# Optimization experiments

Hardware: AMD Instinct MI355X
Metric: run time of the kernel (lower is better)

## Reference

```python
import jax, jax.numpy as jnp
import numpy as np

N = 50000   # nodes
E = 800000  # edges (avg degree 16)
D = 64      # in_feat
OUT = 64    # out_feat


def _layernorm(x, gamma, beta, eps=1e-5):
    m = jnp.mean(x, axis=-1, keepdims=True)
    v = jnp.mean((x - m) ** 2, axis=-1, keepdims=True)  # biased var, as torch LayerNorm
    return (x - m) * jax.lax.rsqrt(v + eps) * gamma + beta


def setup_inputs() -> dict:
    key = jax.random.key(0)
    ks = jax.random.split(key, 6)
    s1 = 1.0 / np.sqrt(D)
    s2 = 1.0 / np.sqrt(2 * D)
    return {
        "x": jax.random.normal(ks[0], (N, D), dtype=jnp.float32),
        "edge_index": jax.random.randint(ks[1], (2, E), 0, N, dtype=jnp.int64),
        "W1a": jax.random.normal(ks[2], (D, D), dtype=jnp.float32) * s1,
        "W1b": jax.random.normal(ks[3], (D, D), dtype=jnp.float32) * s1,
        "gamma1": jnp.ones((D,), jnp.float32),
        "beta1": jnp.zeros((D,), jnp.float32),
        "w": jnp.ones((D,), jnp.float32),
        "gamma2": jnp.ones((D,), jnp.float32),
        "beta2": jnp.zeros((D,), jnp.float32),
        "W2a": jax.random.normal(ks[4], (D, 2 * D), dtype=jnp.float32) * s2,
        "W2b": jax.random.normal(ks[5], (OUT, D), dtype=jnp.float32) * s1,
    }


def reference(x, edge_index, W1a, W1b, gamma1, beta1, w, gamma2, beta2, W2a, W2b):
    row, col = edge_index[0], edge_index[1]
    n = x.shape[0]
    # gather -> MLP1 (two bias-free linears with ReLU)
    msg = x[row]                                        # [E, D]
    msg = jax.nn.relu(msg @ W1a.T) @ W1b.T              # [E, D]
    # scatter_mean over destination nodes
    s = jax.ops.segment_sum(msg, col, num_segments=n)   # [N, D]
    cnt = jax.ops.segment_sum(jnp.ones((col.shape[0],), x.dtype), col, num_segments=n)
    agg = s / jnp.maximum(cnt, 1.0)[:, None]
    agg = _layernorm(agg, gamma1, beta1)
    # repulsion + residual + LayerNorm
    fx = _layernorm(x + (x - agg) * w, gamma2, beta2)
    # concat -> MLP2
    h = jnp.concatenate([fx, agg], axis=1)              # [N, 2D]
    return jax.nn.relu(h @ W2a.T) @ W2b.T               # [N, OUT]
```

## Files before the change

kernel.cpp:

```cpp
#include <hip/hip_runtime.h>
#include <hip/hip_bf16.h>

#define NN 50000
#define NE 800000
#define CAP 48
#define BINS 3125
#define HROW 3126
#define P1B 391
#define CHUNK 2048
#define MLPB 768
#define SUPT 782
#define HIDX(b) ((b) + ((b) >> 4))

typedef short v8s __attribute__((ext_vector_type(8)));
typedef float v4f __attribute__((ext_vector_type(4)));
#define MFMA16(a, b, c) __builtin_amdgcn_mfma_f32_16x16x32_bf16(a, b, c, 0, 0, 0)

__device__ __forceinline__ float bfu2f(unsigned short u) {
    union { unsigned int i; float f; } v; v.i = ((unsigned int)u) << 16; return v.f;
}
__device__ __forceinline__ unsigned short f2bf_rne(float f) {
    union { float f; unsigned int i; } v; v.f = f;
    unsigned int x = v.i;
    unsigned int r = x + 0x7fffu + ((x >> 16) & 1u);
    return (unsigned short)(r >> 16);
}
__device__ __forceinline__ v8s fragf32(const float* p) {
    float4 u = ((const float4*)p)[0];
    float4 v = ((const float4*)p)[1];
    v8s r;
    r[0] = (short)f2bf_rne(u.x); r[1] = (short)f2bf_rne(u.y);
    r[2] = (short)f2bf_rne(u.z); r[3] = (short)f2bf_rne(u.w);
    r[4] = (short)f2bf_rne(v.x); r[5] = (short)f2bf_rne(v.y);
    r[6] = (short)f2bf_rne(v.z); r[7] = (short)f2bf_rne(v.w);
    return r;
}
__device__ __forceinline__ v8s fragbf(const unsigned short* p) {
    union { uint4 u; v8s s; } t; t.u = *((const uint4*)p); return t.s;
}
__device__ __forceinline__ v4f vzero() { v4f z; z[0]=0.f; z[1]=0.f; z[2]=0.f; z[3]=0.f; return z; }

__global__ __launch_bounds__(256) void p1fat_k(const int* __restrict__ ei,
                                               const float* __restrict__ x,
                                               const float* __restrict__ W1a,
                                               const float* __restrict__ W1b,
                                               unsigned int* __restrict__ chunkbuf,
                                               unsigned short* __restrict__ histT,
                                               unsigned short* __restrict__ y) {
    __shared__ __align__(16) unsigned int smem[8448];
    int t = threadIdx.x;
    if (blockIdx.x < P1B) {
        unsigned int*   hcnt  = smem;
        unsigned short* sst16 = (unsigned short*)(smem + 4352);
        unsigned int*   data  = smem + 4352 + 2048;
        unsigned int*   scan  = data;
        int pc = blockIdx.x;
        int e0 = pc * CHUNK;
        int e1 = e0 + CHUNK; if (e1 > NE) e1 = NE;
        int ne = e1 - e0;
        bool i64 = ((ei[1] | ei[3] | ei[5] | ei[7]) == 0);
        for (int i = t; i < 4352; i += 256) hcnt[i] = 0;
        __syncthreads();
        unsigned int packed[8];
#pragma unroll
        for (int i = 0; i < 8; ++i) {
            int e = e0 + t + 256 * i;
            unsigned int pk = 0xFFFFFFFFu;
            if (e < e1) {
                int col = i64 ? ei[2 * (NE + e)] : ei[NE + e];
                int row = i64 ? ei[2 * e]        : ei[e];
                pk = ((unsigned int)col << 16) | (unsigned int)row;
                atomicAdd(&hcnt[HIDX(col >> 4)], 1u);
            }
            packed[i] = pk;
        }
        __syncthreads();
        unsigned int vv[16], tsum = 0;
#pragma unroll
        for (int k = 0; k < 16; ++k) { vv[k] = hcnt[HIDX(16 * t + k)]; tsum += vv[k]; }
        scan[t] = tsum;
        __syncthreads();
        for (int off = 1; off < 256; off <<= 1) {
            unsigned int a = (t >= off) ? scan[t - off] : 0;
            __syncthreads();
            scan[t] += a;
            __syncthreads();
        }
        {
            unsigned int run = scan[t] - tsum;
#pragma unroll
            for (int k = 0; k < 16; ++k) {
                int bb = 16 * t + k;
                hcnt[HIDX(bb)] = run;
                sst16[bb] = (unsigned short)run;
                run += vv[k];
            }
        }
        __syncthreads();
#pragma unroll
        for (int i = 0; i < 8; ++i) {
            unsigned int pk = packed[i];
            if (pk != 0xFFFFFFFFu) {
                unsigned int pos = atomicAdd(&hcnt[HIDX(pk >> 20)], 1u);
                data[pos] = pk;
            }
        }
        __syncthreads();
        unsigned int* cb = chunkbuf + (size_t)pc * CHUNK;
        for (int i = t; i < ne; i += 256) cb[i] = data[i];
        unsigned short* hrow = histT + (size_t)pc * HROW;
        for (int i = t; i < BINS; i += 256) hrow[i] = sst16[i];
        if (t == 0) hrow[BINS] = (unsigned short)ne;
        return;
    }
    unsigned short* wa  = (unsigned short*)smem;
    unsigned short* wb  = wa + 64 * 72;
    unsigned short* h1s = wb + 64 * 72;
    for (int i = t; i < 64 * 64; i += 256) {
        int r = i >> 6, c = i & 63;
        wa[r * 72 + c] = f2bf_rne(W1a[i]);
        wb[r * 72 + c] = f2bf_rne(W1b[i]);
    }
    __syncthreads();
    int w = t >> 6, l = t & 63;
    int lm = l & 15, lq = l >> 4;
    for (int st = blockIdx.x - P1B; st < SUPT; st += MLPB) {
        int nb = st * 64;
        int arow = nb + w * 16 + lm;
        int arc = arow < NN ? arow : NN - 1;
        const float* xr = x + (size_t)arc * 64;
        v8s a0 = fragf32(xr + lq * 8);
        v8s a1 = fragf32(xr + 32 + lq * 8);
        v4f acc[4];
#pragma unroll
        for (int jt = 0; jt < 4; ++jt) acc[jt] = vzero();
#pragma unroll
        for (int jt = 0; jt < 4; ++jt) {
            const unsigned short* wr = &wa[(jt * 16 + lm) * 72];
            acc[jt] = MFMA16(a0, fragbf(wr + lq * 8), acc[jt]);
            acc[jt] = MFMA16(a1, fragbf(wr + 32 + lq * 8), acc[jt]);
        }
#pragma unroll
        for (int jt = 0; jt < 4; ++jt)
#pragma unroll
            for (int r = 0; r < 4; ++r)
                h1s[(w * 16 + lq * 4 + r) * 72 + jt * 16 + lm] = f2bf_rne(fmaxf(acc[jt][r], 0.0f));
        __syncthreads();
        v8s c0 = fragbf(&h1s[(w * 16 + lm) * 72 + lq * 8]);
        v8s c1 = fragbf(&h1s[(w * 16 + lm) * 72 + 32 + lq * 8]);
        v4f acc2[4];
#pragma unroll
        for (int jt = 0; jt < 4; ++jt) acc2[jt] = vzero();
#pragma unroll
        for (int jt = 0; jt < 4; ++jt) {
            const unsigned short* wr = &wb[(jt * 16 + lm) * 72];
            acc2[jt] = MFMA16(c0, fragbf(wr + lq * 8), acc2[jt]);
            acc2[jt] = MFMA16(c1, fragbf(wr + 32 + lq * 8), acc2[jt]);
        }
#pragma unroll
        for (int jt = 0; jt < 4; ++jt)
#pragma unroll
            for (int r = 0; r < 4; ++r) {
                int n = nb + w * 16 + lq * 4 + r;
                if (n < NN) y[(size_t)n * 64 + jt * 16 + lm] = f2bf_rne(acc2[jt][r]);
            }
        __syncthreads();
    }
}

__device__ __forceinline__ float wsum64(float v) {
#pragma unroll
    for (int o = 32; o > 0; o >>= 1) v += __shfl_xor(v, o, 64);
    return v;
}
__device__ __forceinline__ void ln_store(float s0, float s1, int tdeg, int n, int p, int j, int f0,
                                         const float* __restrict__ x,
                                         const float* __restrict__ g1, const float* __restrict__ b1,
                                         const float* __restrict__ wrep,
                                         const float* __restrict__ g2, const float* __restrict__ b2,
                                         unsigned short* hrow) {
    float inv = 1.0f / (float)(tdeg > 1 ? tdeg : 1);
    float a0 = s0 * inv, a1 = s1 * inv;
    float m = wsum64(a0 + a1) * (1.0f / 128.0f);
    float d0 = a0 - m, d1 = a1 - m;
    float var = wsum64(d0 * d0 + d1 * d1) * (1.0f / 128.0f);
    float r = rsqrtf(var + 1e-5f);
    float2 g1v = *(const float2*)(g1 + f0);
    float2 b1v = *(const float2*)(b1 + f0);
    a0 = d0 * r * g1v.x + b1v.x;
    a1 = d1 * r * g1v.y + b1v.y;
    float2 xv = *(const float2*)(x + (size_t)n * 64 + f0);
    float2 wv = *(const float2*)(wrep + f0);
    float t0 = xv.x + (xv.x - a0) * wv.x;
    float t1 = xv.y + (xv.y - a1) * wv.y;
    float m2 = wsum64(t0 + t1) * (1.0f / 128.0f);
    float e0 = t0 - m2, e1 = t1 - m2;
    float var2 = wsum64(e0 * e0 + e1 * e1) * (1.0f / 128.0f);
    float r2 = rsqrtf(var2 + 1e-5f);
    float2 g2v = *(const float2*)(g2 + f0);
    float2 b2v = *(const float2*)(b2 + f0);
    float fx0 = e0 * r2 * g2v.x + b2v.x;
    float fx1 = e1 * r2 * g2v.y + b2v.y;
    unsigned* hw = (unsigned*)hrow;
    if (p == 0) hw[j]      = (unsigned)f2bf_rne(fx0) | ((unsigned)f2bf_rne(fx1) << 16);
    else        hw[32 + j] = (unsigned)f2bf_rne(a0)  | ((unsigned)f2bf_rne(a1)  << 16);
}

__global__ __launch_bounds__(256) void p2gm_k(const unsigned int* __restrict__ chunkbuf,
                                              const unsigned short* __restrict__ histT,
                                              const unsigned short* __restrict__ y,
                                              const float* __restrict__ x,
                                              const float* __restrict__ g1, const float* __restrict__ b1,
                                              const float* __restrict__ wrep,
                                              const float* __restrict__ g2, const float* __restrict__ b2,
                                              const float* __restrict__ W2a,
                                              const float* __restrict__ W2b,
                                              float* __restrict__ out) {
    __shared__ __align__(16) unsigned int k2s[9368];
    unsigned short* wa2 = (unsigned short*)k2s;
    unsigned short* wb2 = wa2 + 64 * 136;
    unsigned short* t2s = wb2 + 64 * 72;
    unsigned short* hs  = t2s + 16 * 72;
    unsigned short* dl  = hs + 16 * 136;
    unsigned int*   cl     = k2s + 8704;
    unsigned int*   scan   = cl + 16;
    unsigned short* sstart = (unsigned short*)(scan + 256);
    unsigned short* sbase  = sstart + 392;
    int t = threadIdx.x;
    int b = blockIdx.x;
    int n0g = b * 16;
    for (int i = t; i < 64 * 128; i += 256) {
        int r = i >> 7, c = i & 127;
        wa2[r * 136 + c] = f2bf_rne(W2a[i]);
    }
    for (int i = t; i < 64 * 64; i += 256) {
        int r = i >> 6, c = i & 63;
        wb2[r * 72 + c] = f2bf_rne(W2b[i]);
    }
    if (t < 16) cl[t] = 0;
    for (int i = t; i < 16 * CAP / 2; i += 256) ((unsigned int*)dl)[i] = 0;
    unsigned l0 = 0, l1 = 0;
    int s0 = 2 * t, s1 = 2 * t + 1;
    if (s0 < P1B) {
        unsigned st = histT[(size_t)s0 * HROW + b], en = histT[(size_t)s0 * HROW + b + 1];
        l0 = en - st; sstart[s0] = (unsigned short)st;
    }
    if (s1 < P1B) {
        unsigned st = histT[(size_t)s1 * HROW + b], en = histT[(size_t)s1 * HROW + b + 1];
        l1 = en - st; sstart[s1] = (unsigned short)st;
    }
    unsigned psum = l0 + l1;
    scan[t] = psum;
    __syncthreads();
    for (int off = 1; off < 256; off <<= 1) {
        unsigned a = (t >= off) ? scan[t - off] : 0;
        __syncthreads();
        scan[t] += a;
        __syncthreads();
    }
    {
        unsigned excl = scan[t] - psum;
        if (s0 < P1B) sbase[s0] = (unsigned short)excl;
        if (s1 < P1B) sbase[s1] = (unsigned short)(excl + l0);
    }
    __syncthreads();
    int tot = (int)scan[255];
    for (int k = t; k < tot; k += 256) {
        int lo = 0, hi = P1B - 1;
#pragma unroll
        for (int it = 0; it < 9; ++it) {
            int mid = (lo + hi + 1) >> 1;
            if ((int)sbase[mid] <= k) lo = mid; else hi = mid - 1;
        }
        int idx = (int)sstart[lo] + (k - (int)sbase[lo]);
        unsigned d = chunkbuf[(size_t)lo * CHUNK + idx];
        int c = (int)(d >> 16) - n0g;
        unsigned slot = atomicAdd(&cl[c], 1u);
        if (slot < CAP) dl[c * CAP + slot] = (unsigned short)(d & 0xffffu);
    }
    __syncthreads();
    int w = t >> 6, l = t & 63;
    int p = l >> 5, j = l & 31, f0 = 2 * j;
#pragma unroll
    for (int q = 0; q < 2; ++q) {
        int nl0 = q * 8 + w * 2, nl1 = nl0 + 1;
        int dA = (int)cl[nl0], dB = (int)cl[nl1];
        int eA = dA < CAP ? dA : CAP;
        int eB = dB < CAP ? dB : CAP;
        float sA0 = 0.f, sA1 = 0.f, sB0 = 0.f, sB1 = 0.f;
#pragma unroll
        for (int c6 = 0; c6 < 6; ++c6) {
            bool cA = c6 * 8 < eA, cB = c6 * 8 < eB;
            if (cA | cB) {
#pragma unroll
                for (int i = 0; i < 4; ++i) {
                    int e = c6 * 8 + 2 * i + p;
                    int idA = (int)dl[nl0 * CAP + e];
                    int idB = (int)dl[nl1 * CAP + e];
                    unsigned uA = *(const unsigned*)(y + (size_t)idA * 64 + f0);
                    unsigned uB = *(const unsigned*)(y + (size_t)idB * 64 + f0);
                    bool okA = cA && e < eA, okB = cB && e < eB;
                    sA0 += okA ? bfu2f((unsigned short)(uA & 0xffffu)) : 0.0f;
                    sA1 += okA ? bfu2f((unsigned short)(uA >> 16)) : 0.0f;
                    sB0 += okB ? bfu2f((unsigned short)(uB & 0xffffu)) : 0.0f;
                    sB1 += okB ? bfu2f((unsigned short)(uB >> 16)) : 0.0f;
                }
            }
        }
        sA0 += __shfl_xor(sA0, 32, 64);
        sA1 += __shfl_xor(sA1, 32, 64);
        sB0 += __shfl_xor(sB0, 32, 64);
        sB1 += __shfl_xor(sB1, 32, 64);
        ln_store(sA0, sA1, dA, n0g + nl0, p, j, f0, x, g1, b1, wrep, g2, b2, hs + nl0 * 136);
        ln_store(sB0, sB1, dB, n0g + nl1, p, j, f0, x, g1, b1, wrep, g2, b2, hs + nl1 * 136);
    }
    __syncthreads();
    int lm = l & 15, lq = l >> 4;
    const unsigned short* fr = hs + lm * 136;
    v8s a0 = fragbf(fr + lq * 8);
    v8s a1 = fragbf(fr + 32 + lq * 8);
    v8s a2 = fragbf(fr + 64 + lq * 8);
    v8s a3 = fragbf(fr + 96 + lq * 8);
    v4f acc = vzero();
    {
        const unsigned short* wr = &wa2[(w * 16 + lm) * 136];
        acc = MFMA16(a0, fragbf(wr + lq * 8), acc);
        acc = MFMA16(a1, fragbf(wr + 32 + lq * 8), acc);
        acc = MFMA16(a2, fragbf(wr + 64 + lq * 8), acc);
        acc = MFMA16(a3, fragbf(wr + 96 + lq * 8), acc);
    }
#pragma unroll
    for (int r = 0; r < 4; ++r)
        t2s[(lq * 4 + r) * 72 + w * 16 + lm] = f2bf_rne(fmaxf(acc[r], 0.0f));
    __syncthreads();
    v8s c0f = fragbf(&t2s[lm * 72 + lq * 8]);
    v8s c1f = fragbf(&t2s[lm * 72 + 32 + lq * 8]);
    v4f acc2 = vzero();
    {
        const unsigned short* wr = &wb2[(w * 16 + lm) * 72];
        acc2 = MFMA16(c0f, fragbf(wr + lq * 8), acc2);
        acc2 = MFMA16(c1f, fragbf(wr + 32 + lq * 8), acc2);
    }
#pragma unroll
    for (int r = 0; r < 4; ++r)
        out[(size_t)(n0g + lq * 4 + r) * 64 + w * 16 + lm] = acc2[r];
}

extern "C" void kernel_launch(void* const* d_in, const int* in_sizes, int n_in,
                              void* d_out, int out_size, void* d_ws, size_t ws_size,
                              hipStream_t stream) {
    const float* x   = (const float*)d_in[0];
    const int*   ei  = (const int*)d_in[1];
    const float* W1a = (const float*)d_in[2];
    const float* W1b = (const float*)d_in[3];
    const float* g1  = (const float*)d_in[4];
    const float* b1  = (const float*)d_in[5];
    const float* w   = (const float*)d_in[6];
    const float* g2  = (const float*)d_in[7];
    const float* b2  = (const float*)d_in[8];
    const float* W2a = (const float*)d_in[9];
    const float* W2b = (const float*)d_in[10];

    char* ws = (char*)d_ws;
    unsigned short* y        = (unsigned short*)(ws + 0);
    unsigned int*   chunkbuf = (unsigned int*)(ws + 6400000);
    unsigned short* histT    = (unsigned short*)(ws + 9603072);

    p1fat_k<<<P1B + MLPB, 256, 0, stream>>>(ei, x, W1a, W1b, chunkbuf, histT, y);
    p2gm_k<<<BINS, 256, 0, stream>>>(chunkbuf, histT, y, x, g1, b1, w, g2, b2,
                                     W2a, W2b, (float*)d_out);
    (void)in_sizes; (void)n_in; (void)out_size; (void)ws_size;
}
```

Before: 152.5 us.

## Split gather+LayerNorm from MLP2 into a separate persistent MFMA kernel

The fused gather/LayerNorm/MLP2 kernel is split in two. The first kernel writes the bf16 concatenated features h, laid out as [N,128], into the output buffer. A second persistent kernel with 768 blocks loads and converts the W2a/W2b weights once per block, then runs both MLP2 matmuls over 64-row tiles, writing fp32 results in place over h. This removes the per-block weight conversion across 3125 blocks and the large LDS footprint from the gather kernel, which should raise its occupancy. The cost is an extra launch and a round trip of h through global memory, and the in-place aliasing relies on each tile reading its own rows before any write.

```diff
diff --git a/kernel.cpp b/kernel.cpp
--- a/kernel.cpp
+++ b/kernel.cpp
@@ -178,7 +178,7 @@
                                          const float* __restrict__ g1, const float* __restrict__ b1,
                                          const float* __restrict__ wrep,
                                          const float* __restrict__ g2, const float* __restrict__ b2,
-                                         unsigned short* hrow) {
+                                         unsigned short* __restrict__ h) {
     float inv = 1.0f / (float)(tdeg > 1 ? tdeg : 1);
     float a0 = s0 * inv, a1 = s1 * inv;
     float m = wsum64(a0 + a1) * (1.0f / 128.0f);
@@ -201,44 +201,30 @@
     float2 b2v = *(const float2*)(b2 + f0);
     float fx0 = e0 * r2 * g2v.x + b2v.x;
     float fx1 = e1 * r2 * g2v.y + b2v.y;
-    unsigned* hw = (unsigned*)hrow;
+    unsigned* hw = (unsigned*)(h + (size_t)n * 128);
     if (p == 0) hw[j]      = (unsigned)f2bf_rne(fx0) | ((unsigned)f2bf_rne(fx1) << 16);
     else        hw[32 + j] = (unsigned)f2bf_rne(a0)  | ((unsigned)f2bf_rne(a1)  << 16);
 }
 
-__global__ __launch_bounds__(256) void p2gm_k(const unsigned int* __restrict__ chunkbuf,
+__global__ __launch_bounds__(256) void p2gl_k(const unsigned int* __restrict__ chunkbuf,
                                               const unsigned short* __restrict__ histT,
                                               const unsigned short* __restrict__ y,
                                               const float* __restrict__ x,
                                               const float* __restrict__ g1, const float* __restrict__ b1,
                                               const float* __restrict__ wrep,
                                               const float* __restrict__ g2, const float* __restrict__ b2,
-                                              const float* __restrict__ W2a,
-                                              const float* __restrict__ W2b,
-                                              float* __restrict__ out) {
-    __shared__ __align__(16) unsigned int k2s[9368];
-    unsigned short* wa2 = (unsigned short*)k2s;
-    unsigned short* wb2 = wa2 + 64 * 136;
-    unsigned short* t2s = wb2 + 64 * 72;
-    unsigned short* hs  = t2s + 16 * 72;
-    unsigned short* dl  = hs + 16 * 136;
-    unsigned int*   cl     = k2s + 8704;
-    unsigned int*   scan   = cl + 16;
-    unsigned short* sstart = (unsigned short*)(scan + 256);
+                                              unsigned short* __restrict__ h) {
+    __shared__ __align__(16) unsigned int s[1048];
+    unsigned short* dl     = (unsigned short*)s;
+    unsigned int*   cl     = s + 384;
+    unsigned int*   scan   = s + 400;
+    unsigned short* sstart = (unsigned short*)(s + 656);
     unsigned short* sbase  = sstart + 392;
     int t = threadIdx.x;
     int b = blockIdx.x;
     int n0g = b * 16;
-    for (int i = t; i < 64 * 128; i += 256) {
-        int r = i >> 7, c = i & 127;
-        wa2[r * 136 + c] = f2bf_rne(W2a[i]);
-    }
-    for (int i = t; i < 64 * 64; i += 256) {
-        int r = i >> 6, c = i & 63;
-        wb2[r * 72 + c] = f2bf_rne(W2b[i]);
-    }
     if (t < 16) cl[t] = 0;
-    for (int i = t; i < 16 * CAP / 2; i += 256) ((unsigned int*)dl)[i] = 0;
+    for (int i = t; i < 384; i += 256) s[i] = 0;
     unsigned l0 = 0, l1 = 0;
     int s0 = 2 * t, s1 = 2 * t + 1;
     if (s0 < P1B) {
@@ -311,39 +297,77 @@
         sA1 += __shfl_xor(sA1, 32, 64);
         sB0 += __shfl_xor(sB0, 32, 64);
         sB1 += __shfl_xor(sB1, 32, 64);
-        ln_store(sA0, sA1, dA, n0g + nl0, p, j, f0, x, g1, b1, wrep, g2, b2, hs + nl0 * 136);
-        ln_store(sB0, sB1, dB, n0g + nl1, p, j, f0, x, g1, b1, wrep, g2, b2, hs + nl1 * 136);
-    }
-    __syncthreads();
+        ln_store(sA0, sA1, dA, n0g + nl0, p, j, f0, x, g1, b1, wrep, g2, b2, h);
+        ln_store(sB0, sB1, dB, n0g + nl1, p, j, f0, x, g1, b1, wrep, g2, b2, h);
+    }
+}
+
+__global__ __launch_bounds__(256) void mlp2_k(const unsigned short* hin,
+                                              const float* __restrict__ W2a,
+                                              const float* __restrict__ W2b,
+                                              float* out) {
+    __shared__ unsigned short sm2[64 * 136 + 64 * 72 + 64 * 72];
+    unsigned short* wa2 = sm2;
+    unsigned short* wb2 = wa2 + 64 * 136;
+    unsigned short* t2s = wb2 + 64 * 72;
+    int t = threadIdx.x;
+    for (int i = t; i < 64 * 128; i += 256) {
+        int r = i >> 7, c = i & 127;
+        wa2[r * 136 + c] = f2bf_rne(W2a[i]);
+    }
+    for (int i = t; i < 64 * 64; i += 256) {
+        int r = i >> 6, c = i & 63;
+        wb2[r * 72 + c] = f2bf_rne(W2b[i]);
+    }
+    __syncthreads();
+    int w = t >> 6, l = t & 63;
     int lm = l & 15, lq = l >> 4;
-    const unsigned short* fr = hs + lm * 136;
-    v8s a0 = fragbf(fr + lq * 8);
-    v8s a1 = fragbf(fr + 32 + lq * 8);
-    v8s a2 = fragbf(fr + 64 + lq * 8);
-    v8s a3 = fragbf(fr + 96 + lq * 8);
-    v4f acc = vzero();
-    {
-        const unsigned short* wr = &wa2[(w * 16 + lm) * 136];
-        acc = MFMA16(a0, fragbf(wr + lq * 8), acc);
-        acc = MFMA16(a1, fragbf(wr + 32 + lq * 8), acc);
-        acc = MFMA16(a2, fragbf(wr + 64 + lq * 8), acc);
-        acc = MFMA16(a3, fragbf(wr + 96 + lq * 8), acc);
-    }
-#pragma unroll
-    for (int r = 0; r < 4; ++r)
-        t2s[(lq * 4 + r) * 72 + w * 16 + lm] = f2bf_rne(fmaxf(acc[r], 0.0f));
-    __syncthreads();
-    v8s c0f = fragbf(&t2s[lm * 72 + lq * 8]);
-    v8s c1f = fragbf(&t2s[lm * 72 + 32 + lq * 8]);
-    v4f acc2 = vzero();
-    {
-        const unsigned short* wr = &wb2[(w * 16 + lm) * 72];
-        acc2 = MFMA16(c0f, fragbf(wr + lq * 8), acc2);
-        acc2 = MFMA16(c1f, fragbf(wr + 32 + lq * 8), acc2);
-    }
-#pragma unroll
-    for (int r = 0; r < 4; ++r)
-        out[(size_t)(n0g + lq * 4 + r) * 64 + w * 16 + lm] = acc2[r];
+    for (int st = blockIdx.x; st < SUPT; st += MLPB) {
+        int nb = st * 64;
+        int arow = nb + w * 16 + lm;
+        int arc = arow < NN ? arow : NN - 1;
+        const unsigned short* fr = hin + (size_t)arc * 128;
+        v8s a0 = fragbf(fr + lq * 8);
+        v8s a1 = fragbf(fr + 32 + lq * 8);
+        v8s a2 = fragbf(fr + 64 + lq * 8);
+        v8s a3 = fragbf(fr + 96 + lq * 8);
+        v4f acc[4];
+#pragma unroll
+        for (int jt = 0; jt < 4; ++jt) acc[jt] = vzero();
+#pragma unroll
+        for (int jt = 0; jt < 4; ++jt) {
+            const unsigned short* wr = &wa2[(jt * 16 + lm) * 136];
+            acc[jt] = MFMA16(a0, fragbf(wr + lq * 8), acc[jt]);
+            acc[jt] = MFMA16(a1, fragbf(wr + 32 + lq * 8), acc[jt]);
+            acc[jt] = MFMA16(a2, fragbf(wr + 64 + lq * 8), acc[jt]);
+            acc[jt] = MFMA16(a3, fragbf(wr + 96 + lq * 8), acc[jt]);
+        }
+#pragma unroll
+        for (int jt = 0; jt < 4; ++jt)
+#pragma unroll
+            for (int r = 0; r < 4; ++r)
+                t2s[(w * 16 + lq * 4 + r) * 72 + jt * 16 + lm] = f2bf_rne(fmaxf(acc[jt][r], 0.0f));
+        __syncthreads();
+        v8s c0 = fragbf(&t2s[(w * 16 + lm) * 72 + lq * 8]);
+        v8s c1 = fragbf(&t2s[(w * 16 + lm) * 72 + 32 + lq * 8]);
+        v4f acc2[4];
+#pragma unroll
+        for (int jt = 0; jt < 4; ++jt) acc2[jt] = vzero();
+#pragma unroll
+        for (int jt = 0; jt < 4; ++jt) {
+            const unsigned short* wr = &wb2[(jt * 16 + lm) * 72];
+            acc2[jt] = MFMA16(c0, fragbf(wr + lq * 8), acc2[jt]);
+            acc2[jt] = MFMA16(c1, fragbf(wr + 32 + lq * 8), acc2[jt]);
+        }
+#pragma unroll
+        for (int jt = 0; jt < 4; ++jt)
+#pragma unroll
+            for (int r = 0; r < 4; ++r) {
+                int n = nb + w * 16 + lq * 4 + r;
+                if (n < NN) out[(size_t)n * 64 + jt * 16 + lm] = acc2[jt][r];
+            }
+        __syncthreads();
+    }
 }
 
 extern "C" void kernel_launch(void* const* d_in, const int* in_sizes, int n_in,
@@ -367,7 +391,8 @@
     unsigned short* histT    = (unsigned short*)(ws + 9603072);
 
     p1fat_k<<<P1B + MLPB, 256, 0, stream>>>(ei, x, W1a, W1b, chunkbuf, histT, y);
-    p2gm_k<<<BINS, 256, 0, stream>>>(chunkbuf, histT, y, x, g1, b1, w, g2, b2,
-                                     W2a, W2b, (float*)d_out);
+    p2gl_k<<<BINS, 256, 0, stream>>>(chunkbuf, histT, y, x, g1, b1, w, g2, b2,
+                                     (unsigned short*)d_out);
+    mlp2_k<<<MLPB, 256, 0, stream>>>((const unsigned short*)d_out, W2a, W2b, (float*)d_out);
     (void)in_sizes; (void)n_in; (void)out_size; (void)ws_size;
 }
```

Result: faster. 138.6 us (-9.1%).

## Load MLP2 weights into registers and simplify edge bucketing in gather kernel

Applied to the files above, without the earlier changes.

The second kernel stops staging the converted W2a/W2b matrices in shared memory. Each lane now loads its MFMA weight fragments straight from global fp32 into registers, which cuts LDS from about 37KB to about 8KB per block and should allow more resident blocks. The prefix-scan plus binary-search distribution of chunk entries is replaced by a simple per-thread loop over each segment's range. Unused slots in the neighbour lists are filled with a sentinel id (50000) that points at zeroed padding rows of y, so the per-edge validity masks in the gather loop can be dropped. The per-thread segment loop may be less load-balanced, and the padding rows shift the workspace offsets.

```diff
diff --git a/kernel.cpp b/kernel.cpp
--- a/kernel.cpp
+++ b/kernel.cpp
@@ -2,6 +2,7 @@
 #include <hip/hip_bf16.h>
 
 #define NN 50000
+#define NYR 50048
 #define NE 800000
 #define CAP 48
 #define BINS 3125
@@ -162,7 +163,8 @@
 #pragma unroll
             for (int r = 0; r < 4; ++r) {
                 int n = nb + w * 16 + lq * 4 + r;
-                if (n < NN) y[(size_t)n * 64 + jt * 16 + lm] = f2bf_rne(acc2[jt][r]);
+                y[(size_t)n * 64 + jt * 16 + lm] = (n < NN) ? f2bf_rne(acc2[jt][r])
+                                                            : (unsigned short)0;
             }
         __syncthreads();
     }
@@ -178,7 +180,7 @@
                                          const float* __restrict__ g1, const float* __restrict__ b1,
                                          const float* __restrict__ wrep,
                                          const float* __restrict__ g2, const float* __restrict__ b2,
-                                         unsigned short* hrow) {
+                                         unsigned* hw) {
     float inv = 1.0f / (float)(tdeg > 1 ? tdeg : 1);
     float a0 = s0 * inv, a1 = s1 * inv;
     float m = wsum64(a0 + a1) * (1.0f / 128.0f);
@@ -201,85 +203,53 @@
     float2 b2v = *(const float2*)(b2 + f0);
     float fx0 = e0 * r2 * g2v.x + b2v.x;
     float fx1 = e1 * r2 * g2v.y + b2v.y;
-    unsigned* hw = (unsigned*)hrow;
     if (p == 0) hw[j]      = (unsigned)f2bf_rne(fx0) | ((unsigned)f2bf_rne(fx1) << 16);
     else        hw[32 + j] = (unsigned)f2bf_rne(a0)  | ((unsigned)f2bf_rne(a1)  << 16);
 }
 
-__global__ __launch_bounds__(256) void p2gm_k(const unsigned int* __restrict__ chunkbuf,
-                                              const unsigned short* __restrict__ histT,
-                                              const unsigned short* __restrict__ y,
-                                              const float* __restrict__ x,
-                                              const float* __restrict__ g1, const float* __restrict__ b1,
-                                              const float* __restrict__ wrep,
-                                              const float* __restrict__ g2, const float* __restrict__ b2,
-                                              const float* __restrict__ W2a,
-                                              const float* __restrict__ W2b,
-                                              float* __restrict__ out) {
-    __shared__ __align__(16) unsigned int k2s[9368];
-    unsigned short* wa2 = (unsigned short*)k2s;
-    unsigned short* wb2 = wa2 + 64 * 136;
-    unsigned short* t2s = wb2 + 64 * 72;
-    unsigned short* hs  = t2s + 16 * 72;
-    unsigned short* dl  = hs + 16 * 136;
-    unsigned int*   cl     = k2s + 8704;
-    unsigned int*   scan   = cl + 16;
-    unsigned short* sstart = (unsigned short*)(scan + 256);
-    unsigned short* sbase  = sstart + 392;
+__global__ __launch_bounds__(256) void p2glm_k(const unsigned int* __restrict__ chunkbuf,
+                                               const unsigned short* __restrict__ histT,
+                                               const unsigned short* __restrict__ y,
+                                               const float* __restrict__ x,
+                                               const float* __restrict__ g1, const float* __restrict__ b1,
+                                               const float* __restrict__ wrep,
+                                               const float* __restrict__ g2, const float* __restrict__ b2,
+                                               const float* __restrict__ W2a,
+                                               const float* __restrict__ W2b,
+                                               float* __restrict__ out) {
+    __shared__ __align__(16) unsigned int s[2064];
+    unsigned short* dl  = (unsigned short*)s;
+    unsigned int*   cl  = s + 384;
+    unsigned short* hs  = (unsigned short*)(s + 400);
+    unsigned short* t2s = (unsigned short*)(s + 1488);
     int t = threadIdx.x;
     int b = blockIdx.x;
     int n0g = b * 16;
-    for (int i = t; i < 64 * 128; i += 256) {
-        int r = i >> 7, c = i & 127;
-        wa2[r * 136 + c] = f2bf_rne(W2a[i]);
-    }
-    for (int i = t; i < 64 * 64; i += 256) {
-        int r = i >> 6, c = i & 63;
-        wb2[r * 72 + c] = f2bf_rne(W2b[i]);
-    }
+    int w = t >> 6, l = t & 63;
+    int lm = l & 15, lq = l >> 4;
+    const float* wra = W2a + (size_t)(w * 16 + lm) * 128;
+    v8s qa0 = fragf32(wra + lq * 8);
+    v8s qa1 = fragf32(wra + 32 + lq * 8);
+    v8s qa2 = fragf32(wra + 64 + lq * 8);
+    v8s qa3 = fragf32(wra + 96 + lq * 8);
+    const float* wrb = W2b + (size_t)(w * 16 + lm) * 64;
+    v8s qb0 = fragf32(wrb + lq * 8);
+    v8s qb1 = fragf32(wrb + 32 + lq * 8);
     if (t < 16) cl[t] = 0;
-    for (int i = t; i < 16 * CAP / 2; i += 256) ((unsigned int*)dl)[i] = 0;
-    unsigned l0 = 0, l1 = 0;
-    int s0 = 2 * t, s1 = 2 * t + 1;
-    if (s0 < P1B) {
-        unsigned st = histT[(size_t)s0 * HROW + b], en = histT[(size_t)s0 * HROW + b + 1];
-        l0 = en - st; sstart[s0] = (unsigned short)st;
-    }
-    if (s1 < P1B) {
-        unsigned st = histT[(size_t)s1 * HROW + b], en = histT[(size_t)s1 * HROW + b + 1];
-        l1 = en - st; sstart[s1] = (unsigned short)st;
-    }
-    unsigned psum = l0 + l1;
-    scan[t] = psum;
-    __syncthreads();
-    for (int off = 1; off < 256; off <<= 1) {
-        unsigned a = (t >= off) ? scan[t - off] : 0;
-        __syncthreads();
-        scan[t] += a;
-        __syncthreads();
-    }
-    {
-        unsigned excl = scan[t] - psum;
-        if (s0 < P1B) sbase[s0] = (unsigned short)excl;
-        if (s1 < P1B) sbase[s1] = (unsigned short)(excl + l0);
-    }
-    __syncthreads();
-    int tot = (int)scan[255];
-    for (int k = t; k < tot; k += 256) {
-        int lo = 0, hi = P1B - 1;
-#pragma unroll
-        for (int it = 0; it < 9; ++it) {
-            int mid = (lo + hi + 1) >> 1;
-            if ((int)sbase[mid] <= k) lo = mid; else hi = mid - 1;
-        }
-        int idx = (int)sstart[lo] + (k - (int)sbase[lo]);
-        unsigned d = chunkbuf[(size_t)lo * CHUNK + idx];
-        int c = (int)(d >> 16) - n0g;
-        unsigned slot = atomicAdd(&cl[c], 1u);
-        if (slot < CAP) dl[c * CAP + slot] = (unsigned short)(d & 0xffffu);
-    }
-    __syncthreads();
-    int w = t >> 6, l = t & 63;
+    for (int i = t; i < 384; i += 256) s[i] = 0xC350C350u;
+    __syncthreads();
+    for (int sg = t; sg < P1B; sg += 256) {
+        int st = (int)histT[(size_t)sg * HROW + b];
+        int en = (int)histT[(size_t)sg * HROW + b + 1];
+        const unsigned int* cb = chunkbuf + (size_t)sg * CHUNK;
+        for (int i = st; i < en; ++i) {
+            unsigned d = cb[i];
+            int c = (int)(d >> 16) - n0g;
+            unsigned slot = atomicAdd(&cl[c], 1u);
+            if (slot < CAP) dl[c * CAP + slot] = (unsigned short)(d & 0xffffu);
+        }
+    }
+    __syncthreads();
     int p = l >> 5, j = l & 31, f0 = 2 * j;
 #pragma unroll
     for (int q = 0; q < 2; ++q) {
@@ -299,11 +269,10 @@
                     int idB = (int)dl[nl1 * CAP + e];
                     unsigned uA = *(const unsigned*)(y + (size_t)idA * 64 + f0);
                     unsigned uB = *(const unsigned*)(y + (size_t)idB * 64 + f0);
-                    bool okA = cA && e < eA, okB = cB && e < eB;
-                    sA0 += okA ? bfu2f((unsigned short)(uA & 0xffffu)) : 0.0f;
-                    sA1 += okA ? bfu2f((unsigned short)(uA >> 16)) : 0.0f;
-                    sB0 += okB ? bfu2f((unsigned short)(uB & 0xffffu)) : 0.0f;
-                    sB1 += okB ? bfu2f((unsigned short)(uB >> 16)) : 0.0f;
+                    sA0 += bfu2f((unsigned short)(uA & 0xffffu));
+                    sA1 += bfu2f((unsigned short)(uA >> 16));
+                    sB0 += bfu2f((unsigned short)(uB & 0xffffu));
+                    sB1 += bfu2f((unsigned short)(uB >> 16));
                 }
             }
         }
@@ -311,24 +280,22 @@
         sA1 += __shfl_xor(sA1, 32, 64);
         sB0 += __shfl_xor(sB0, 32, 64);
         sB1 += __shfl_xor(sB1, 32, 64);
-        ln_store(sA0, sA1, dA, n0g + nl0, p, j, f0, x, g1, b1, wrep, g2, b2, hs + nl0 * 136);
-        ln_store(sB0, sB1, dB, n0g + nl1, p, j, f0, x, g1, b1, wrep, g2, b2, hs + nl1 * 136);
-    }
-    __syncthreads();
-    int lm = l & 15, lq = l >> 4;
+        ln_store(sA0, sA1, dA, n0g + nl0, p, j, f0, x, g1, b1, wrep, g2, b2,
+                 (unsigned*)(hs + nl0 * 136));
+        ln_store(sB0, sB1, dB, n0g + nl1, p, j, f0, x, g1, b1, wrep, g2, b2,
+                 (unsigned*)(hs + nl1 * 136));
+    }
+    __syncthreads();
     const unsigned short* fr = hs + lm * 136;
     v8s a0 = fragbf(fr + lq * 8);
     v8s a1 = fragbf(fr + 32 + lq * 8);
     v8s a2 = fragbf(fr + 64 + lq * 8);
     v8s a3 = fragbf(fr + 96 + lq * 8);
     v4f acc = vzero();
-    {
-        const unsigned short* wr = &wa2[(w * 16 + lm) * 136];
-        acc = MFMA16(a0, fragbf(wr + lq * 8), acc);
-        acc = MFMA16(a1, fragbf(wr + 32 + lq * 8), acc);
-        acc = MFMA16(a2, fragbf(wr + 64 + lq * 8), acc);
-        acc = MFMA16(a3, fragbf(wr + 96 + lq * 8), acc);
-    }
+    acc = MFMA16(a0, qa0, acc);
+    acc = MFMA16(a1, qa1, acc);
+    acc = MFMA16(a2, qa2, acc);
+    acc = MFMA16(a3, qa3, acc);
 #pragma unroll
     for (int r = 0; r < 4; ++r)
         t2s[(lq * 4 + r) * 72 + w * 16 + lm] = f2bf_rne(fmaxf(acc[r], 0.0f));
@@ -336,11 +303,8 @@
     v8s c0f = fragbf(&t2s[lm * 72 + lq * 8]);
     v8s c1f = fragbf(&t2s[lm * 72 + 32 + lq * 8]);
     v4f acc2 = vzero();
-    {
-        const unsigned short* wr = &wb2[(w * 16 + lm) * 72];
-        acc2 = MFMA16(c0f, fragbf(wr + lq * 8), acc2);
-        acc2 = MFMA16(c1f, fragbf(wr + 32 + lq * 8), acc2);
-    }
+    acc2 = MFMA16(c0f, qb0, acc2);
+    acc2 = MFMA16(c1f, qb1, acc2);
 #pragma unroll
     for (int r = 0; r < 4; ++r)
         out[(size_t)(n0g + lq * 4 + r) * 64 + w * 16 + lm] = acc2[r];
@@ -363,11 +327,11 @@
 
     char* ws = (char*)d_ws;
     unsigned short* y        = (unsigned short*)(ws + 0);
-    unsigned int*   chunkbuf = (unsigned int*)(ws + 6400000);
-    unsigned short* histT    = (unsigned short*)(ws + 9603072);
+    unsigned int*   chunkbuf = (unsigned int*)(ws + 6406144);
+    unsigned short* histT    = (unsigned short*)(ws + 9609216);
 
     p1fat_k<<<P1B + MLPB, 256, 0, stream>>>(ei, x, W1a, W1b, chunkbuf, histT, y);
-    p2gm_k<<<BINS, 256, 0, stream>>>(chunkbuf, histT, y, x, g1, b1, w, g2, b2,
-                                     W2a, W2b, (float*)d_out);
+    p2glm_k<<<BINS, 256, 0, stream>>>(chunkbuf, histT, y, x, g1, b1, w, g2, b2,
+                                      W2a, W2b, (float*)d_out);
     (void)in_sizes; (void)n_in; (void)out_size; (void)ws_size;
 }
```

New measurement: 154.3 us. No clear change (+1.2%).
